# Kernel optimization log

Hardware: AMD Instinct MI355X
Metric: run time of the kernel (lower is better)

The kernel has to match this reference:

```python
import jax, jax.numpy as jnp
import numpy as np

KH, KW = 3, 3      # kernel_size
SH, SW = 1, 1      # stride
MINVAL, MAXVAL = -0.45, -0.15


def setup_inputs() -> dict:
    key = jax.random.key(0)
    kx, kw = jax.random.split(key)
    x = jax.random.normal(kx, (16, 128, 128, 16), dtype=jnp.float32)  # NHWC
    W = jax.random.uniform(kw, (KH, KW, 16, 32), minval=MINVAL, maxval=MAXVAL,
                           dtype=jnp.float32)  # [kh, kw, C_in, filters]
    return {"x": x, "W": W}


def _dilation(x, W):
    # Max-plus sliding-window 'convolution' (VALID padding):
    # out[b,i,j,f] = max_{di,dj,c} x[b, i*SH+di, j*SW+dj, c] + W[di,dj,c,f]
    kh, kw, C, F = W.shape
    B, H, Wd, _ = x.shape
    Hout = (H - kh) // SH + 1
    Wout = (Wd - kw) // SW + 1
    out = jnp.full((B, Hout, Wout, F), -jnp.inf, dtype=x.dtype)
    for di in range(kh):          # small fixed loop over kernel offsets
        for dj in range(kw):
            xs = x[:, di:di + Hout * SH:SH, dj:dj + Wout * SW:SW, :]  # [B,Hout,Wout,C]
            # add W for this offset, reduce max over input channels
            out = jnp.maximum(out, jnp.max(xs[..., :, None] + W[di, dj], axis=3))
    return out


def reference(x, W):
    # erosion(x) = -dilation(-x)
    return -_dilation(-x, W)
```

## Files before the change

kernel.cpp:

```cpp
#include <hip/hip_runtime.h>
#include <math.h>


#define TI 21
#define TROWS (TI + 2)
#define LROW 64

typedef _Float16 h2 __attribute__((ext_vector_type(2)));

__device__ __forceinline__ h2 hmin2(h2 a, h2 b) {
    return __builtin_elementwise_min(a, b);
}

__device__ __forceinline__ h2 pkrtz(float a, float b) {
    auto r = __builtin_amdgcn_cvt_pkrtz(a, b);
    return *reinterpret_cast<h2*>(&r);
}

__device__ __forceinline__ h2 rowmin3(const float4* pr, const h2 w[3][4]) {
    h2 t[12];
#pragma unroll
    for (int dj = 0; dj < 3; ++dj) {
        const h2* p = reinterpret_cast<const h2*>(&pr[dj]);
#pragma unroll
        for (int q = 0; q < 4; ++q)
            t[dj * 4 + q] = p[q] - w[dj][q];
    }
#pragma unroll
    for (int k = 0; k < 6; ++k) t[k] = hmin2(t[k], t[k + 6]);
    t[0] = hmin2(t[0], t[3]);
    t[1] = hmin2(t[1], t[4]);
    t[2] = hmin2(t[2], t[5]);
    return hmin2(hmin2(t[0], t[1]), t[2]);
}

__global__ __launch_bounds__(256) void erosion_kernel(
    const float* __restrict__ x, const float* __restrict__ Wt,
    float* __restrict__ out)
{
    __shared__ _Float16 tile[2 * TROWS * LROW];
    __shared__ _Float16 vmbuf[TI * 256];

    const int tid = threadIdx.x;
    const int f  = tid & 31;
    const int ch = (tid >> 5) & 1;
    const int jt = tid >> 6;
    const int b  = blockIdx.z;
    const int i0 = blockIdx.y * TI;
    const int jb = blockIdx.x * 4;

    {
        const float* xg = x + (size_t)b * (128 * 128 * 16);
        auto stage = [&](int t) {
            int r   = t / 12;
            int k   = t % 12;
            int cc  = k >> 1;
            int ch2 = k & 1;
            int col = min(jb + cc, 127);
            const float* src = xg + ((size_t)(i0 + r) * 128 + col) * 16 + ch2 * 8;
            float4 lo = *reinterpret_cast<const float4*>(src);
            float4 hi = *reinterpret_cast<const float4*>(src + 4);
            h2 o[4] = { pkrtz(lo.x, lo.y), pkrtz(lo.z, lo.w),
                        pkrtz(hi.x, hi.y), pkrtz(hi.z, hi.w) };
            *reinterpret_cast<float4*>(
                &tile[ch2 * (TROWS * LROW) + r * LROW + cc * 8]) =
                *reinterpret_cast<float4*>(o);
        };
        stage(tid);
        if (tid < TROWS * 12 - 256) stage(tid + 256);
    }

    h2 wh[3][3][4];
#pragma unroll
    for (int di = 0; di < 3; ++di)
#pragma unroll
        for (int dj = 0; dj < 3; ++dj)
#pragma unroll
            for (int q = 0; q < 4; ++q) {
                int p = di * 3 + dj;
                float a = Wt[(p * 16 + ch * 8 + 2 * q) * 32 + f];
                float c = Wt[(p * 16 + ch * 8 + 2 * q + 1) * 32 + f];
                wh[di][dj][q] = pkrtz(a, c);
            }

    __syncthreads();

    const _Float16* lb = &tile[ch * (TROWS * LROW) + jt * 8];

    const _Float16 HINF = (_Float16)__builtin_huge_valf();
    h2 accB = {HINF, HINF};
    h2 accC = {HINF, HINF};

    float4 pre[3];
#pragma unroll
    for (int dj = 0; dj < 3; ++dj)
        pre[dj] = *reinterpret_cast<const float4*>(lb + dj * 8);

    auto body = [&](int r, bool do_prefetch, bool do_vm) {
        h2 n0 = rowmin3(pre, wh[0]);
        h2 n1 = rowmin3(pre, wh[1]);
        h2 n2 = rowmin3(pre, wh[2]);

        if (do_prefetch) {
            const _Float16* ln = lb + (r + 1) * LROW;
#pragma unroll
            for (int dj = 0; dj < 3; ++dj)
                pre[dj] = *reinterpret_cast<const float4*>(ln + dj * 8);
        }

        h2 fin2 = hmin2(accC, n2);
        accC = hmin2(accB, n1);
        accB = n0;

        if (do_vm) {
            _Float16 a = fin2[0], c = fin2[1];
            _Float16 vm = a < c ? a : c;
            vmbuf[(r - 2) * 256 + tid] = vm;
        }
    };

    body(0, true, false);
    body(1, true, false);
#pragma unroll 2
    for (int r = 2; r < TROWS - 1; ++r)
        body(r, true, true);
    body(TROWS - 1, false, true);

    __syncthreads();

    {
        float* outb = out + (size_t)b * (126 * 126 * 32);
        auto merge = [&](int t) {
            int row = t >> 5;
            int k   = t & 31;
            int col = k >> 3;
            int q   = k & 7;
            int jj  = jb + col;
            const _Float16* base = &vmbuf[row * 256 + col * 64 + q * 4];
            h2 a[2], c[2];
            *reinterpret_cast<double*>(a) = *reinterpret_cast<const double*>(base);
            *reinterpret_cast<double*>(c) = *reinterpret_cast<const double*>(base + 32);
            h2 m0 = hmin2(a[0], c[0]);
            h2 m1 = hmin2(a[1], c[1]);
            float4 o = { (float)m0[0], (float)m0[1], (float)m1[0], (float)m1[1] };
            if (jj < 126)
                *reinterpret_cast<float4*>(
                    &outb[((size_t)(i0 + row) * 126 + jj) * 32 + q * 4]) = o;
        };
        merge(tid);
        merge(tid + 256);
        if (tid < TI * 32 - 512) merge(tid + 512);
    }
}

extern "C" void kernel_launch(void* const* d_in, const int* in_sizes, int n_in,
                              void* d_out, int out_size, void* d_ws, size_t ws_size,
                              hipStream_t stream) {
    const float* x  = (const float*)d_in[0];
    const float* Wt = (const float*)d_in[1];
    float* out = (float*)d_out;

    dim3 grid(32, 6, 16);
    dim3 block(256);
    erosion_kernel<<<grid, block, 0, stream>>>(x, Wt, out);
}
```

Baseline: 109.2 us.

## Compute two output columns per thread and store directly via cross-lane shuffle

Each thread now computes two adjacent output columns, sharing overlapping input row loads from shared memory, and the block tile widens to eight columns with half as many blocks. The shared-memory staging buffer and the separate merge pass are replaced by a wave shuffle that combines the two channel halves, followed by direct scalar global stores. This aims to cut shared-memory traffic, a barrier and the epilogue. In exchange, stores become scalar with half the lanes idle and the grid has fewer blocks.

```diff
diff --git a/kernel.cpp b/kernel.cpp
--- a/kernel.cpp
+++ b/kernel.cpp
@@ -4,7 +4,8 @@
 
 #define TI 21
 #define TROWS (TI + 2)
-#define LROW 64
+#define TCOLS 10
+#define LROW 96
 
 typedef _Float16 h2 __attribute__((ext_vector_type(2)));
 
@@ -39,7 +40,6 @@
     float* __restrict__ out)
 {
     __shared__ _Float16 tile[2 * TROWS * LROW];
-    __shared__ _Float16 vmbuf[TI * 256];
 
     const int tid = threadIdx.x;
     const int f  = tid & 31;
@@ -47,13 +47,16 @@
     const int jt = tid >> 6;
     const int b  = blockIdx.z;
     const int i0 = blockIdx.y * TI;
-    const int jb = blockIdx.x * 4;
+    const int jb = blockIdx.x * 8;
+    const int j0 = jb + 2 * jt;
+    const bool w0 = (ch == 0) && (j0     < 126);
+    const bool w1 = (ch == 0) && (j0 + 1 < 126);
 
     {
         const float* xg = x + (size_t)b * (128 * 128 * 16);
         auto stage = [&](int t) {
-            int r   = t / 12;
-            int k   = t % 12;
+            int r   = t / 20;
+            int k   = t % 20;
             int cc  = k >> 1;
             int ch2 = k & 1;
             int col = min(jb + cc, 127);
@@ -67,7 +70,7 @@
                 *reinterpret_cast<float4*>(o);
         };
         stage(tid);
-        if (tid < TROWS * 12 - 256) stage(tid + 256);
+        if (tid < TROWS * 20 - 256) stage(tid + 256);
     }
 
     h2 wh[3][3][4];
@@ -85,37 +88,48 @@
 
     __syncthreads();
 
-    const _Float16* lb = &tile[ch * (TROWS * LROW) + jt * 8];
+    const _Float16* lb = &tile[ch * (TROWS * LROW) + (2 * jt) * 8];
+    float* op = out + (((size_t)b * 126 + i0) * 126 + j0) * 32 + f;
 
     const _Float16 HINF = (_Float16)__builtin_huge_valf();
-    h2 accB = {HINF, HINF};
-    h2 accC = {HINF, HINF};
+    h2 accB0 = {HINF, HINF}, accB1 = {HINF, HINF};
+    h2 accC0 = {HINF, HINF}, accC1 = {HINF, HINF};
 
-    float4 pre[3];
+    float4 pre[4];
 #pragma unroll
-    for (int dj = 0; dj < 3; ++dj)
-        pre[dj] = *reinterpret_cast<const float4*>(lb + dj * 8);
+    for (int s = 0; s < 4; ++s)
+        pre[s] = *reinterpret_cast<const float4*>(lb + s * 8);
 
-    auto body = [&](int r, bool do_prefetch, bool do_vm) {
-        h2 n0 = rowmin3(pre, wh[0]);
-        h2 n1 = rowmin3(pre, wh[1]);
-        h2 n2 = rowmin3(pre, wh[2]);
+    auto body = [&](int r, bool do_prefetch, bool do_store) {
+        h2 n00 = rowmin3(&pre[0], wh[0]);
+        h2 n01 = rowmin3(&pre[0], wh[1]);
+        h2 n02 = rowmin3(&pre[0], wh[2]);
+        h2 n10 = rowmin3(&pre[1], wh[0]);
+        h2 n11 = rowmin3(&pre[1], wh[1]);
+        h2 n12 = rowmin3(&pre[1], wh[2]);
 
         if (do_prefetch) {
             const _Float16* ln = lb + (r + 1) * LROW;
 #pragma unroll
-            for (int dj = 0; dj < 3; ++dj)
-                pre[dj] = *reinterpret_cast<const float4*>(ln + dj * 8);
+            for (int s = 0; s < 4; ++s)
+                pre[s] = *reinterpret_cast<const float4*>(ln + s * 8);
         }
 
-        h2 fin2 = hmin2(accC, n2);
-        accC = hmin2(accB, n1);
-        accB = n0;
+        h2 fin0 = hmin2(accC0, n02);
+        h2 fin1 = hmin2(accC1, n12);
+        accC0 = hmin2(accB0, n01);  accB0 = n00;
+        accC1 = hmin2(accB1, n11);  accB1 = n10;
 
-        if (do_vm) {
-            _Float16 a = fin2[0], c = fin2[1];
-            _Float16 vm = a < c ? a : c;
-            vmbuf[(r - 2) * 256 + tid] = vm;
+        if (do_store) {
+            _Float16 a0 = fin0[0], c0 = fin0[1];
+            _Float16 a1 = fin1[0], c1 = fin1[1];
+            float v0 = (float)(a0 < c0 ? a0 : c0);
+            float v1 = (float)(a1 < c1 ? a1 : c1);
+            v0 = fminf(v0, __shfl_xor(v0, 32));
+            v1 = fminf(v1, __shfl_xor(v1, 32));
+            float* row = op + (size_t)(r - 2) * (126 * 32);
+            if (w0) row[0]  = v0;
+            if (w1) row[32] = v1;
         }
     };
 
@@ -125,32 +139,6 @@
     for (int r = 2; r < TROWS - 1; ++r)
         body(r, true, true);
     body(TROWS - 1, false, true);
-
-    __syncthreads();
-
-    {
-        float* outb = out + (size_t)b * (126 * 126 * 32);
-        auto merge = [&](int t) {
-            int row = t >> 5;
-            int k   = t & 31;
-            int col = k >> 3;
-            int q   = k & 7;
-            int jj  = jb + col;
-            const _Float16* base = &vmbuf[row * 256 + col * 64 + q * 4];
-            h2 a[2], c[2];
-            *reinterpret_cast<double*>(a) = *reinterpret_cast<const double*>(base);
-            *reinterpret_cast<double*>(c) = *reinterpret_cast<const double*>(base + 32);
-            h2 m0 = hmin2(a[0], c[0]);
-            h2 m1 = hmin2(a[1], c[1]);
-            float4 o = { (float)m0[0], (float)m0[1], (float)m1[0], (float)m1[1] };
-            if (jj < 126)
-                *reinterpret_cast<float4*>(
-                    &outb[((size_t)(i0 + row) * 126 + jj) * 32 + q * 4]) = o;
-        };
-        merge(tid);
-        merge(tid + 256);
-        if (tid < TI * 32 - 512) merge(tid + 512);
-    }
 }
 
 extern "C" void kernel_launch(void* const* d_in, const int* in_sizes, int n_in,
@@ -160,7 +148,7 @@
     const float* Wt = (const float*)d_in[1];
     float* out = (float*)d_out;
 
-    dim3 grid(32, 6, 16);
+    dim3 grid(16, 6, 16);
     dim3 block(256);
     erosion_kernel<<<grid, block, 0, stream>>>(x, Wt, out);
 }
```

New measurement: 111.7 us. +2.2%, slower.

## Store outputs directly with cross-half shuffle and use taller row tiles

Applied to the files above, without the earlier changes.

Replaces the shared-memory vmbuf staging and the cooperative merge/write phase with a direct per-row global store. The two channel halves are combined with a lane shuffle, and only one half writes. The row tile grows from 21 to 32 rows, with the last block overlapped at row 94, so the grid drops to 4 row blocks. This removes a barrier and the LDS round trip, and it amortizes the halo and weight loads over more rows. In exchange, each store is a scalar 4-byte write per lane, and half the lanes sit idle at every store.

```diff
diff --git a/kernel.cpp b/kernel.cpp
--- a/kernel.cpp
+++ b/kernel.cpp
@@ -2,7 +2,7 @@
 #include <math.h>
 
 
-#define TI 21
+#define TI 32
 #define TROWS (TI + 2)
 #define LROW 64
 
@@ -39,15 +39,19 @@
     float* __restrict__ out)
 {
     __shared__ _Float16 tile[2 * TROWS * LROW];
-    __shared__ _Float16 vmbuf[TI * 256];
 
     const int tid = threadIdx.x;
     const int f  = tid & 31;
     const int ch = (tid >> 5) & 1;
     const int jt = tid >> 6;
     const int b  = blockIdx.z;
-    const int i0 = blockIdx.y * TI;
+    const int by = blockIdx.y;
+    const int i0 = (by == 3) ? 94 : by * TI;
     const int jb = blockIdx.x * 4;
+    int j = jb + jt;
+    const bool jvalid = (j < 126);
+    if (!jvalid) j = 125;
+    const bool writer = jvalid && (ch == 0);
 
     {
         const float* xg = x + (size_t)b * (128 * 128 * 16);
@@ -86,6 +90,7 @@
     __syncthreads();
 
     const _Float16* lb = &tile[ch * (TROWS * LROW) + jt * 8];
+    float* op = out + (((size_t)b * 126 + i0) * 126 + j) * 32 + f;
 
     const _Float16 HINF = (_Float16)__builtin_huge_valf();
     h2 accB = {HINF, HINF};
@@ -96,7 +101,7 @@
     for (int dj = 0; dj < 3; ++dj)
         pre[dj] = *reinterpret_cast<const float4*>(lb + dj * 8);
 
-    auto body = [&](int r, bool do_prefetch, bool do_vm) {
+    auto body = [&](int r, bool do_prefetch, bool do_store) {
         h2 n0 = rowmin3(pre, wh[0]);
         h2 n1 = rowmin3(pre, wh[1]);
         h2 n2 = rowmin3(pre, wh[2]);
@@ -112,10 +117,12 @@
         accC = hmin2(accB, n1);
         accB = n0;
 
-        if (do_vm) {
+        if (do_store) {
             _Float16 a = fin2[0], c = fin2[1];
-            _Float16 vm = a < c ? a : c;
-            vmbuf[(r - 2) * 256 + tid] = vm;
+            float v = (float)(a < c ? a : c);
+            v = fminf(v, __shfl_xor(v, 32));
+            if (writer)
+                op[(size_t)(r - 2) * (126 * 32)] = v;
         }
     };
 
@@ -125,32 +132,6 @@
     for (int r = 2; r < TROWS - 1; ++r)
         body(r, true, true);
     body(TROWS - 1, false, true);
-
-    __syncthreads();
-
-    {
-        float* outb = out + (size_t)b * (126 * 126 * 32);
-        auto merge = [&](int t) {
-            int row = t >> 5;
-            int k   = t & 31;
-            int col = k >> 3;
-            int q   = k & 7;
-            int jj  = jb + col;
-            const _Float16* base = &vmbuf[row * 256 + col * 64 + q * 4];
-            h2 a[2], c[2];
-            *reinterpret_cast<double*>(a) = *reinterpret_cast<const double*>(base);
-            *reinterpret_cast<double*>(c) = *reinterpret_cast<const double*>(base + 32);
-            h2 m0 = hmin2(a[0], c[0]);
-            h2 m1 = hmin2(a[1], c[1]);
-            float4 o = { (float)m0[0], (float)m0[1], (float)m1[0], (float)m1[1] };
-            if (jj < 126)
-                *reinterpret_cast<float4*>(
-                    &outb[((size_t)(i0 + row) * 126 + jj) * 32 + q * 4]) = o;
-        };
-        merge(tid);
-        merge(tid + 256);
-        if (tid < TI * 32 - 512) merge(tid + 512);
-    }
 }
 
 extern "C" void kernel_launch(void* const* d_in, const int* in_sizes, int n_in,
@@ -160,7 +141,7 @@
     const float* Wt = (const float*)d_in[1];
     float* out = (float*)d_out;
 
-    dim3 grid(32, 6, 16);
+    dim3 grid(32, 4, 16);
     dim3 block(256);
     erosion_kernel<<<grid, block, 0, stream>>>(x, Wt, out);
 }
```

Result: no change. 110.8 us (+1.4%).
